# Optimization experiments

Hardware: AMD Instinct MI355X
Metric: run time of the kernel (lower is better)

Reference implementation:

```python
import jax, jax.numpy as jnp
import numpy as np

N = 100000   # nodes
E = 1600000  # edges
F = 128      # node features
H = 64       # hidden_dim
G = 64       # graphs in batch


def setup_inputs() -> dict:
    key = jax.random.key(0)
    ks = jax.random.split(key, 12)
    x = jax.random.normal(ks[0], (N, F), jnp.float32)
    edge_index = jax.random.randint(ks[1], (2, E), 0, N, dtype=jnp.int64)
    batch = jnp.sort(jax.random.randint(ks[2], (N,), 0, G, dtype=jnp.int64))
    s = 0.05
    W1 = jax.random.normal(ks[3], (F, H), jnp.float32) * s
    b1 = jnp.zeros((H,), jnp.float32)
    W2 = jax.random.normal(ks[4], (H, H), jnp.float32) * s
    b2 = jnp.zeros((H,), jnp.float32)
    Wa = jax.random.normal(ks[5], (H, 1), jnp.float32) * s
    ba = jnp.zeros((1,), jnp.float32)
    Wc = jax.random.normal(ks[6], (H, 1), jnp.float32) * s
    bc = jnp.zeros((1,), jnp.float32)
    return {"x": x, "edge_index": edge_index, "batch": batch,
            "W1": W1, "b1": b1, "W2": W2, "b2": b2,
            "Wa": Wa, "ba": ba, "Wc": Wc, "bc": bc}


def _gcn_norm(edge_index, n):
    # Add self-loops, compute symmetric normalization deg^-1/2[src]*deg^-1/2[dst]
    loop = jnp.arange(n, dtype=edge_index.dtype)
    src = jnp.concatenate([edge_index[0], loop])
    dst = jnp.concatenate([edge_index[1], loop])
    deg = jax.ops.segment_sum(jnp.ones_like(src, jnp.float32), dst, num_segments=n)
    dinv = jnp.where(deg > 0, deg ** -0.5, 0.0)
    norm = dinv[src] * dinv[dst]  # [E+N]
    return src, dst, norm


def _gcn_conv(x, W, b, src, dst, norm, n):
    h = x @ W                         # [n, H] dense transform first (PyG order)
    msg = h[src] * norm[:, None]      # gather + normalize [E+n, H]
    agg = jax.ops.segment_sum(msg, dst, num_segments=n)  # scatter-add
    return agg + b


def reference(x, edge_index, batch, W1, b1, W2, b2, Wa, ba, Wc, bc):
    n = x.shape[0]
    src, dst, norm = _gcn_norm(edge_index, n)
    h = jax.nn.relu(_gcn_conv(x, W1, b1, src, dst, norm, n))
    # dropout p=0.1 is identity in eval mode
    h = jax.nn.relu(_gcn_conv(h, W2, b2, src, dst, norm, n))
    action_logits = (h @ Wa + ba)[:, 0]  # [N]
    counts = jax.ops.segment_sum(jnp.ones((n,), jnp.float32), batch, num_segments=G)
    pooled = jax.ops.segment_sum(h, batch, num_segments=G) / jnp.maximum(counts, 1.0)[:, None]
    value = pooled @ Wc + bc  # [G, 1]
    return action_logits, value
```

## Files before the change

kernel.cpp:

```cpp
#include <hip/hip_runtime.h>
#include <hip/hip_fp16.h>
#include <math.h>

#define FEAT 128
#define HID  64
#define BSH  7
#define BNODES (1 << BSH)
#define PB   256
#define SRCM ((1u << 25) - 1)
#define PSPLIT 16

typedef _Float16 f16_t;
typedef f16_t half8 __attribute__((ext_vector_type(8)));
typedef float  f32x4 __attribute__((ext_vector_type(4)));


__global__ void part_hist_k(const int* __restrict__ dst, int* __restrict__ table,
                            int e, int nb) {
    __shared__ int lcnt[1024];
    for (int i = threadIdx.x; i < nb; i += 256) lcnt[i] = 0;
    __syncthreads();
    int eb = (e + PB - 1) / PB;
    int lo = blockIdx.x * eb, hi = min(lo + eb, e);
    for (int i = lo + threadIdx.x; i < hi; i += 256)
        atomicAdd(&lcnt[dst[i] >> BSH], 1);
    __syncthreads();
    for (int k = threadIdx.x; k < nb; k += 256)
        table[k * PB + blockIdx.x] = lcnt[k];
}

__global__ void scan1_k(int* __restrict__ data, int* __restrict__ aux, int L) {
    __shared__ int s[1024];
    int gid = blockIdx.x * 1024 + threadIdx.x;
    int v = (gid < L) ? data[gid] : 0;
    s[threadIdx.x] = v;
    __syncthreads();
    for (int off = 1; off < 1024; off <<= 1) {
        int t = (threadIdx.x >= off) ? s[threadIdx.x - off] : 0;
        __syncthreads();
        s[threadIdx.x] += t;
        __syncthreads();
    }
    if (gid < L) data[gid] = s[threadIdx.x] - v;
    if (threadIdx.x == 1023) aux[blockIdx.x] = s[1023];
}

__global__ void scan2_k(int* aux, int naux) {
    __shared__ int s[1024];
    int v = (threadIdx.x < naux) ? aux[threadIdx.x] : 0;
    s[threadIdx.x] = v;
    __syncthreads();
    for (int off = 1; off < 1024; off <<= 1) {
        int t = (threadIdx.x >= off) ? s[threadIdx.x - off] : 0;
        __syncthreads();
        s[threadIdx.x] += t;
        __syncthreads();
    }
    if (threadIdx.x < naux) aux[threadIdx.x] = s[threadIdx.x] - v;
}

__global__ void part_scatter_k(const int* __restrict__ src, const int* __restrict__ dst,
                               const int* __restrict__ table, const int* __restrict__ aux,
                               unsigned* __restrict__ packed, int e, int nb) {
    __shared__ int loff[1024];
    for (int k = threadIdx.x; k < nb; k += 256) {
        int idx = k * PB + blockIdx.x;
        loff[k] = table[idx] + aux[idx >> 10];
    }
    __syncthreads();
    int eb = (e + PB - 1) / PB;
    int lo = blockIdx.x * eb, hi = min(lo + eb, e);
    for (int i = lo + threadIdx.x; i < hi; i += 256) {
        int d = dst[i];
        int p = atomicAdd(&loff[d >> BSH], 1);
        packed[p] = ((unsigned)(d & (BNODES - 1)) << 25) | (unsigned)src[i];
    }
}


__global__ void bucket_sort_k(const unsigned* __restrict__ packed,
                              const int* __restrict__ table, const int* __restrict__ aux,
                              int* __restrict__ col, int* __restrict__ rowptr,
                              float* __restrict__ dinv, int n, int e, int nb) {
    __shared__ int cnt[BNODES];
    __shared__ int s[BNODES];
    __shared__ int cur[BNODES];
    const int k = blockIdx.x;
    const int t = threadIdx.x;
    if (t < BNODES) cnt[t] = 0;
    __syncthreads();
    int i0 = k * PB;
    int i1 = (k + 1) * PB;
    const int bs = table[i0] + aux[i0 >> 10];
    const int be = (k + 1 < nb) ? (table[i1] + aux[i1 >> 10]) : e;
    for (int i = bs + t; i < be; i += 256)
        atomicAdd(&cnt[packed[i] >> 25], 1);
    __syncthreads();
    if (t < BNODES) s[t] = cnt[t];
    __syncthreads();
    for (int off = 1; off < BNODES; off <<= 1) {
        int v = (t < BNODES && t >= off) ? s[t - off] : 0;
        __syncthreads();
        if (t < BNODES) s[t] += v;
        __syncthreads();
    }
    if (t < BNODES) {
        int base = bs + s[t] - cnt[t];
        cur[t] = base;
        int node = (k << BSH) + t;
        if (node < n) {
            rowptr[node] = base;
            dinv[node] = 1.0f / sqrtf(1.0f + (float)cnt[t]);
            if (node == n - 1) rowptr[n] = base + cnt[t];
        }
    }
    __syncthreads();
    for (int i = bs + t; i < be; i += 256) {
        unsigned u = packed[i];
        int p = atomicAdd(&cur[u >> 25], 1);
        col[p] = (int)(u & SRCM);
    }
}


__global__ __launch_bounds__(256, 3)
void gemm_tile_k(const float* __restrict__ X, const float* __restrict__ W,
                 const float* __restrict__ dinv, __half* __restrict__ out, int n) {
    constexpr int K = FEAT;
    __shared__ float sX[64][K + 4];
    __shared__ float sW[64][64];
    const int row0 = blockIdx.x * 64;
    const int t  = threadIdx.x;
    const int tx = t & 15;
    const int ty = t >> 4;

    const float* xb = X + (size_t)row0 * K;
#pragma unroll
    for (int it = 0; it < K / 16; ++it) {
        int fl = it * 1024 + t * 4;
        int r  = fl >> 7;
        int k  = fl & (K - 1);
        float4 v = make_float4(0.f, 0.f, 0.f, 0.f);
        if (row0 + r < n) v = *(const float4*)(xb + fl);
        *(float4*)&sX[r][k] = v;
    }

    float acc[4][4] = {};
#pragma unroll
    for (int ph = 0; ph < K / 64; ++ph) {
        __syncthreads();
#pragma unroll
        for (int it = 0; it < 4; ++it) {
            int fl = it * 1024 + t * 4;
            *(float4*)&sW[fl >> 6][fl & 63] = *(const float4*)(W + ph * 64 * HID + fl);
        }
        __syncthreads();

#pragma unroll 8
        for (int k = 0; k < 64; k += 4) {
            float4 a[4], b[4];
#pragma unroll
            for (int i = 0; i < 4; i++) a[i] = *(float4*)&sX[ty * 4 + i][ph * 64 + k];
#pragma unroll
            for (int j = 0; j < 4; j++) b[j] = *(float4*)&sW[k + j][tx * 4];
#pragma unroll
            for (int i = 0; i < 4; i++) {
                acc[i][0] = fmaf(a[i].x, b[0].x, acc[i][0]);
                acc[i][1] = fmaf(a[i].x, b[0].y, acc[i][1]);
                acc[i][2] = fmaf(a[i].x, b[0].z, acc[i][2]);
                acc[i][3] = fmaf(a[i].x, b[0].w, acc[i][3]);
                acc[i][0] = fmaf(a[i].y, b[1].x, acc[i][0]);
                acc[i][1] = fmaf(a[i].y, b[1].y, acc[i][1]);
                acc[i][2] = fmaf(a[i].y, b[1].z, acc[i][2]);
                acc[i][3] = fmaf(a[i].y, b[1].w, acc[i][3]);
                acc[i][0] = fmaf(a[i].z, b[2].x, acc[i][0]);
                acc[i][1] = fmaf(a[i].z, b[2].y, acc[i][1]);
                acc[i][2] = fmaf(a[i].z, b[2].z, acc[i][2]);
                acc[i][3] = fmaf(a[i].z, b[2].w, acc[i][3]);
                acc[i][0] = fmaf(a[i].w, b[3].x, acc[i][0]);
                acc[i][1] = fmaf(a[i].w, b[3].y, acc[i][1]);
                acc[i][2] = fmaf(a[i].w, b[3].z, acc[i][2]);
                acc[i][3] = fmaf(a[i].w, b[3].w, acc[i][3]);
            }
        }
    }

#pragma unroll
    for (int i = 0; i < 4; i++) {
        int gr = row0 + ty * 4 + i;
        if (gr < n) {
            float sc = dinv[gr];
            union { __half2 h[2]; unsigned long long u; } pk;
            pk.h[0] = __floats2half2_rn(acc[i][0] * sc, acc[i][1] * sc);
            pk.h[1] = __floats2half2_rn(acc[i][2] * sc, acc[i][3] * sc);
            *(unsigned long long*)(out + (size_t)gr * HID + tx * 4) = pk.u;
        }
    }
}


__global__ void gather1_k(const __half* __restrict__ tS, const int* __restrict__ rowptr,
                          const int* __restrict__ col, const float* __restrict__ dinv,
                          const float* __restrict__ b, __half* __restrict__ out, int n) {
    int node = (int)((blockIdx.x * (size_t)blockDim.x + threadIdx.x) >> 5);
    int lane = threadIdx.x & 31;
    if (node >= n) return;
    int beg = rowptr[node], end = rowptr[node + 1];
    const __half2* tl = (const __half2*)tS + lane;
    float2 acc = __half22float2(tl[node * 32]);
    int e = beg;
    for (; e + 16 <= end; e += 16) {
        int s[16];
        __half2 v[16];
#pragma unroll
        for (int j = 0; j < 16; j++) s[j] = col[e + j];
#pragma unroll
        for (int j = 0; j < 16; j++) v[j] = tl[s[j] * 32];
        float2 t0 = make_float2(0.f, 0.f), t1 = make_float2(0.f, 0.f);
#pragma unroll
        for (int j = 0; j < 8; j++) {
            float2 f = __half22float2(v[j]);
            t0.x += f.x; t0.y += f.y;
        }
#pragma unroll
        for (int j = 8; j < 16; j++) {
            float2 f = __half22float2(v[j]);
            t1.x += f.x; t1.y += f.y;
        }
        acc.x += t0.x + t1.x;
        acc.y += t0.y + t1.y;
    }
    for (; e + 4 <= end; e += 4) {
        __half2 v0 = tl[col[e] * 32];
        __half2 v1 = tl[col[e + 1] * 32];
        __half2 v2 = tl[col[e + 2] * 32];
        __half2 v3 = tl[col[e + 3] * 32];
        float2 f0 = __half22float2(v0), f1 = __half22float2(v1);
        float2 f2 = __half22float2(v2), f3 = __half22float2(v3);
        acc.x += (f0.x + f1.x) + (f2.x + f3.x);
        acc.y += (f0.y + f1.y) + (f2.y + f3.y);
    }
    for (; e < end; ++e) {
        float2 f = __half22float2(tl[col[e] * 32]);
        acc.x += f.x; acc.y += f.y;
    }
    float d = dinv[node];
    float2 bb = *(const float2*)(b + 2 * lane);
    float h0 = fmaxf(fmaf(d, acc.x, bb.x), 0.0f);
    float h1 = fmaxf(fmaf(d, acc.y, bb.y), 0.0f);
    ((__half2*)out)[node * 32 + lane] = __floats2half2_rn(h0, h1);
}


__global__ __launch_bounds__(256)
void t2_k(const __half* __restrict__ h, const float* __restrict__ W2,
          const float* __restrict__ dinv, __half* __restrict__ out, int n) {
    const int wave  = threadIdx.x >> 6;
    const int l     = threadIdx.x & 63;
    const int strip = blockIdx.x * 4 + wave;
    const int r0    = strip * 16;
    if (r0 >= n) return;
    const int col = l & 15;
    const int kb  = l >> 4;

    half8 bf[4][2];
#pragma unroll
    for (int t = 0; t < 4; ++t)
#pragma unroll
        for (int kk = 0; kk < 2; ++kk)
#pragma unroll
            for (int j = 0; j < 8; ++j)
                bf[t][kk][j] = (f16_t)W2[(kk * 32 + kb * 8 + j) * HID + t * 16 + col];

    const int arow = r0 + col;
    const __half* ap = h + (size_t)arow * HID + kb * 8;
    half8 a0 = *(const half8*)(ap);
    half8 a1 = *(const half8*)(ap + 32);

    f32x4 acc[4] = {};
#pragma unroll
    for (int t = 0; t < 4; ++t) {
        acc[t] = __builtin_amdgcn_mfma_f32_16x16x32_f16(a0, bf[t][0], acc[t], 0, 0, 0);
        acc[t] = __builtin_amdgcn_mfma_f32_16x16x32_f16(a1, bf[t][1], acc[t], 0, 0, 0);
    }

    const int rbase = r0 + kb * 4;
#pragma unroll
    for (int r = 0; r < 4; ++r) {
        int gr = rbase + r;
        if (gr < n) {
            float dv = dinv[gr];
#pragma unroll
            for (int t = 0; t < 4; ++t)
                out[(size_t)gr * HID + t * 16 + col] = __float2half(acc[t][r] * dv);
        }
    }
}


__global__ void gather2_k(const __half* __restrict__ tS, const int* __restrict__ rowptr,
                          const int* __restrict__ col, const float* __restrict__ dinv,
                          const float* __restrict__ b, __half* __restrict__ out,
                          const float* __restrict__ Wa, const float* __restrict__ ba,
                          float* __restrict__ logits, int n) {
    int node = (int)((blockIdx.x * (size_t)blockDim.x + threadIdx.x) >> 5);
    int lane = threadIdx.x & 31;
    if (node >= n) return;
    int beg = rowptr[node], end = rowptr[node + 1];
    const __half2* tl = (const __half2*)tS + lane;
    float2 acc = __half22float2(tl[node * 32]);
    int e = beg;
    for (; e + 16 <= end; e += 16) {
        int s[16];
        __half2 v[16];
#pragma unroll
        for (int j = 0; j < 16; j++) s[j] = col[e + j];
#pragma unroll
        for (int j = 0; j < 16; j++) v[j] = tl[s[j] * 32];
        float2 t0 = make_float2(0.f, 0.f), t1 = make_float2(0.f, 0.f);
#pragma unroll
        for (int j = 0; j < 8; j++) {
            float2 f = __half22float2(v[j]);
            t0.x += f.x; t0.y += f.y;
        }
#pragma unroll
        for (int j = 8; j < 16; j++) {
            float2 f = __half22float2(v[j]);
            t1.x += f.x; t1.y += f.y;
        }
        acc.x += t0.x + t1.x;
        acc.y += t0.y + t1.y;
    }
    for (; e + 4 <= end; e += 4) {
        __half2 v0 = tl[col[e] * 32];
        __half2 v1 = tl[col[e + 1] * 32];
        __half2 v2 = tl[col[e + 2] * 32];
        __half2 v3 = tl[col[e + 3] * 32];
        float2 f0 = __half22float2(v0), f1 = __half22float2(v1);
        float2 f2 = __half22float2(v2), f3 = __half22float2(v3);
        acc.x += (f0.x + f1.x) + (f2.x + f3.x);
        acc.y += (f0.y + f1.y) + (f2.y + f3.y);
    }
    for (; e < end; ++e) {
        float2 f = __half22float2(tl[col[e] * 32]);
        acc.x += f.x; acc.y += f.y;
    }
    float d = dinv[node];
    float2 bb = *(const float2*)(b + 2 * lane);
    float h0 = fmaxf(fmaf(d, acc.x, bb.x), 0.0f);
    float h1 = fmaxf(fmaf(d, acc.y, bb.y), 0.0f);
    ((__half2*)out)[node * 32 + lane] = __floats2half2_rn(h0, h1);
    float2 wa = *(const float2*)(Wa + 2 * lane);
    float p = h0 * wa.x + h1 * wa.y;
#pragma unroll
    for (int off = 16; off > 0; off >>= 1) p += __shfl_down(p, off, 32);
    if (lane == 0) logits[node] = p + ba[0];
}


__global__ void pool2_k(const __half* __restrict__ h, const int* __restrict__ batch,
                        float* __restrict__ pooled, int n) {
    const int gid  = blockIdx.x / PSPLIT;
    const int part = blockIdx.x % PSPLIT;
    int lo = 0, hi = n;
    while (lo < hi) { int m = (lo + hi) >> 1; if (batch[m] < gid) lo = m + 1; else hi = m; }
    const int b0 = lo;
    hi = n;
    while (lo < hi) { int m = (lo + hi) >> 1; if (batch[m] < gid + 1) lo = m + 1; else hi = m; }
    const int b1 = lo;
    const int chunk = (b1 - b0 + PSPLIT - 1) / PSPLIT;
    const int r0 = b0 + part * chunk;
    const int r1 = min(r0 + chunk, b1);
    const int lane = threadIdx.x & 31;
    const int rg   = threadIdx.x >> 5;
    const __half2* hp = (const __half2*)h + lane;
    float2 acc = make_float2(0.f, 0.f);
    for (int i = r0 + rg; i < r1; i += 8) {
        float2 f = __half22float2(hp[(size_t)i * 32]);
        acc.x += f.x; acc.y += f.y;
    }
    __shared__ float2 red[8][32];
    red[rg][lane] = acc;
    __syncthreads();
    if (threadIdx.x < 32) {
        float2 s = make_float2(0.f, 0.f);
#pragma unroll
        for (int r = 0; r < 8; r++) { s.x += red[r][threadIdx.x].x; s.y += red[r][threadIdx.x].y; }
        atomicAdd(&pooled[gid * HID + 2 * threadIdx.x], s.x);
        atomicAdd(&pooled[gid * HID + 2 * threadIdx.x + 1], s.y);
    }
}


__global__ void value_k(const float* __restrict__ pooled, const int* __restrict__ batch,
                        const float* __restrict__ Wc, const float* __restrict__ bc,
                        float* __restrict__ val, int n, int g) {
    int gw   = (int)((blockIdx.x * (size_t)blockDim.x + threadIdx.x) >> 6);
    int lane = threadIdx.x & 63;
    if (gw >= g) return;
    int lo = 0, hi = n;
    while (lo < hi) { int m = (lo + hi) >> 1; if (batch[m] < gw) lo = m + 1; else hi = m; }
    int b0 = lo;
    lo = 0; hi = n;
    while (lo < hi) { int m = (lo + hi) >> 1; if (batch[m] < gw + 1) lo = m + 1; else hi = m; }
    float cnt = fmaxf((float)(lo - b0), 1.0f);
    float p = (pooled[gw * HID + lane] / cnt) * Wc[lane];
#pragma unroll
    for (int off = 32; off > 0; off >>= 1) p += __shfl_down(p, off);
    if (lane == 0) val[gw] = p + bc[0];
}

extern "C" void kernel_launch(void* const* d_in, const int* in_sizes, int n_in,
                              void* d_out, int out_size, void* d_ws, size_t ws_size,
                              hipStream_t stream) {
    const float* x     = (const float*)d_in[0];
    const int*   ei    = (const int*)d_in[1];
    const int*   batch = (const int*)d_in[2];
    const float* W1    = (const float*)d_in[3];
    const float* b1    = (const float*)d_in[4];
    const float* W2    = (const float*)d_in[5];
    const float* b2    = (const float*)d_in[6];
    const float* Wa    = (const float*)d_in[7];
    const float* ba    = (const float*)d_in[8];
    const float* Wc    = (const float*)d_in[9];
    const float* bc    = (const float*)d_in[10];

    const int n = in_sizes[0] / FEAT;
    const int e = in_sizes[1] / 2;
    const int g = out_size - n;
    const int* src = ei;
    const int* dst = ei + e;

    const int nb = (n + BNODES - 1) >> BSH;
    const int L  = nb * PB;

    float*    ws     = (float*)d_ws;
    float*    dinv   = ws;
    float*    bufA   = dinv + n;
    float*    bufB   = bufA + (size_t)n * HID;
    float*    pooled = bufB + (size_t)n * HID;
    int*      table  = (int*)(pooled + (size_t)g * HID);
    int*      aux    = table + L;
    int*      rowptr = aux + 1024;
    int*      col    = rowptr + n + 1;
    unsigned* packed = (unsigned*)bufA;
    __half*   tS1    = (__half*)bufA;
    __half*   h16    = (__half*)bufB;
    __half*   tS2    = (__half*)bufA;
    __half*   h2     = (__half*)bufB;

    const int B = 256;
    const int gridT  = (n + 63) / 64;
    const int gridG  = (int)(((size_t)n * 32 + B - 1) / B);
    const int strips = (n + 15) / 16;
    const int gridT2 = (strips + 3) / 4;
    const int nb1    = (L + 1023) / 1024;

    (void)hipMemsetAsync(pooled, 0, (size_t)g * HID * sizeof(float), stream);

    part_hist_k<<<PB, B, 0, stream>>>(dst, table, e, nb);
    scan1_k<<<nb1, 1024, 0, stream>>>(table, aux, L);
    scan2_k<<<1, 1024, 0, stream>>>(aux, nb1);
    part_scatter_k<<<PB, B, 0, stream>>>(src, dst, table, aux, packed, e, nb);
    bucket_sort_k<<<nb, B, 0, stream>>>(packed, table, aux, col, rowptr, dinv, n, e, nb);

    gemm_tile_k<<<gridT, B, 0, stream>>>(x, W1, dinv, tS1, n);
    gather1_k<<<gridG, B, 0, stream>>>(tS1, rowptr, col, dinv, b1, h16, n);

    t2_k<<<gridT2, B, 0, stream>>>(h16, W2, dinv, tS2, n);
    gather2_k<<<gridG, B, 0, stream>>>(tS2, rowptr, col, dinv, b2, h2,
                                       Wa, ba, (float*)d_out, n);

    pool2_k<<<g * PSPLIT, B, 0, stream>>>(h2, batch, pooled, n);
    value_k<<<(g * 64 + B - 1) / B, B, 0, stream>>>(pooled, batch, Wc, bc,
                                                    (float*)d_out + n, n, g);
}
```

Before: 296.6 us.

## Replace two-level bucket CSR build with global-atomic counting sort

Replaces the partitioned histogram, bucket scatter and per-bucket local sort with a simpler CSR build: global atomic degree counting, a scan over n nodes, a finalize kernel for rowptr/dinv, and a scatter using global atomics on per-node cursors. It drops the packed intermediate pass and the local-memory sort, at the cost of 1.6M contended global atomics in two passes and fully random col writes. Column order within a row becomes nondeterministic, which can change float summation order.

```diff
diff --git a/kernel.cpp b/kernel.cpp
--- a/kernel.cpp
+++ b/kernel.cpp
@@ -4,10 +4,6 @@
 
 #define FEAT 128
 #define HID  64
-#define BSH  7
-#define BNODES (1 << BSH)
-#define PB   256
-#define SRCM ((1u << 25) - 1)
 #define PSPLIT 16
 
 typedef _Float16 f16_t;
@@ -15,18 +11,11 @@
 typedef float  f32x4 __attribute__((ext_vector_type(4)));
 
 
-__global__ void part_hist_k(const int* __restrict__ dst, int* __restrict__ table,
-                            int e, int nb) {
-    __shared__ int lcnt[1024];
-    for (int i = threadIdx.x; i < nb; i += 256) lcnt[i] = 0;
-    __syncthreads();
-    int eb = (e + PB - 1) / PB;
-    int lo = blockIdx.x * eb, hi = min(lo + eb, e);
-    for (int i = lo + threadIdx.x; i < hi; i += 256)
-        atomicAdd(&lcnt[dst[i] >> BSH], 1);
-    __syncthreads();
-    for (int k = threadIdx.x; k < nb; k += 256)
-        table[k * PB + blockIdx.x] = lcnt[k];
+__global__ void deg_k(const int* __restrict__ dst, int* __restrict__ deg, int e) {
+    int i = blockIdx.x * 256 + threadIdx.x;
+    int stride = gridDim.x * 256;
+    for (; i < e; i += stride)
+        atomicAdd(&deg[dst[i]], 1);
 }
 
 __global__ void scan1_k(int* __restrict__ data, int* __restrict__ aux, int L) {
@@ -59,66 +48,26 @@
     if (threadIdx.x < naux) aux[threadIdx.x] = s[threadIdx.x] - v;
 }
 
-__global__ void part_scatter_k(const int* __restrict__ src, const int* __restrict__ dst,
-                               const int* __restrict__ table, const int* __restrict__ aux,
-                               unsigned* __restrict__ packed, int e, int nb) {
-    __shared__ int loff[1024];
-    for (int k = threadIdx.x; k < nb; k += 256) {
-        int idx = k * PB + blockIdx.x;
-        loff[k] = table[idx] + aux[idx >> 10];
-    }
-    __syncthreads();
-    int eb = (e + PB - 1) / PB;
-    int lo = blockIdx.x * eb, hi = min(lo + eb, e);
-    for (int i = lo + threadIdx.x; i < hi; i += 256) {
-        int d = dst[i];
-        int p = atomicAdd(&loff[d >> BSH], 1);
-        packed[p] = ((unsigned)(d & (BNODES - 1)) << 25) | (unsigned)src[i];
-    }
-}
-
-
-__global__ void bucket_sort_k(const unsigned* __restrict__ packed,
-                              const int* __restrict__ table, const int* __restrict__ aux,
-                              int* __restrict__ col, int* __restrict__ rowptr,
-                              float* __restrict__ dinv, int n, int e, int nb) {
-    __shared__ int cnt[BNODES];
-    __shared__ int s[BNODES];
-    __shared__ int cur[BNODES];
-    const int k = blockIdx.x;
-    const int t = threadIdx.x;
-    if (t < BNODES) cnt[t] = 0;
-    __syncthreads();
-    int i0 = k * PB;
-    int i1 = (k + 1) * PB;
-    const int bs = table[i0] + aux[i0 >> 10];
-    const int be = (k + 1 < nb) ? (table[i1] + aux[i1 >> 10]) : e;
-    for (int i = bs + t; i < be; i += 256)
-        atomicAdd(&cnt[packed[i] >> 25], 1);
-    __syncthreads();
-    if (t < BNODES) s[t] = cnt[t];
-    __syncthreads();
-    for (int off = 1; off < BNODES; off <<= 1) {
-        int v = (t < BNODES && t >= off) ? s[t - off] : 0;
-        __syncthreads();
-        if (t < BNODES) s[t] += v;
-        __syncthreads();
-    }
-    if (t < BNODES) {
-        int base = bs + s[t] - cnt[t];
-        cur[t] = base;
-        int node = (k << BSH) + t;
-        if (node < n) {
-            rowptr[node] = base;
-            dinv[node] = 1.0f / sqrtf(1.0f + (float)cnt[t]);
-            if (node == n - 1) rowptr[n] = base + cnt[t];
-        }
-    }
-    __syncthreads();
-    for (int i = bs + t; i < be; i += 256) {
-        unsigned u = packed[i];
-        int p = atomicAdd(&cur[u >> 25], 1);
-        col[p] = (int)(u & SRCM);
+__global__ void fin_k(const int* __restrict__ sc, const int* __restrict__ aux,
+                      int* __restrict__ rowptr, int* __restrict__ cur,
+                      float* __restrict__ dinv, int n, int e) {
+    int i = blockIdx.x * 256 + threadIdx.x;
+    if (i >= n) return;
+    int rp = sc[i] + aux[i >> 10];
+    rowptr[i] = rp;
+    cur[i] = rp;
+    int next = (i + 1 < n) ? (sc[i + 1] + aux[(i + 1) >> 10]) : e;
+    dinv[i] = 1.0f / sqrtf(1.0f + (float)(next - rp));
+    if (i == n - 1) rowptr[n] = e;
+}
+
+__global__ void scat_k(const int* __restrict__ src, const int* __restrict__ dst,
+                       int* __restrict__ cur, int* __restrict__ col, int e) {
+    int i = blockIdx.x * 256 + threadIdx.x;
+    int stride = gridDim.x * 256;
+    for (; i < e; i += stride) {
+        int p = atomicAdd(&cur[dst[i]], 1);
+        col[p] = src[i];
     }
 }
 
@@ -431,19 +380,16 @@
     const int* src = ei;
     const int* dst = ei + e;
 
-    const int nb = (n + BNODES - 1) >> BSH;
-    const int L  = nb * PB;
-
     float*    ws     = (float*)d_ws;
     float*    dinv   = ws;
     float*    bufA   = dinv + n;
     float*    bufB   = bufA + (size_t)n * HID;
     float*    pooled = bufB + (size_t)n * HID;
-    int*      table  = (int*)(pooled + (size_t)g * HID);
-    int*      aux    = table + L;
+    int*      deg    = (int*)(pooled + (size_t)g * HID);
+    int*      aux    = deg + n;
     int*      rowptr = aux + 1024;
-    int*      col    = rowptr + n + 1;
-    unsigned* packed = (unsigned*)bufA;
+    int*      cur    = rowptr + n + 1;
+    int*      col    = cur + n;
     __half*   tS1    = (__half*)bufA;
     __half*   h16    = (__half*)bufB;
     __half*   tS2    = (__half*)bufA;
@@ -454,15 +400,16 @@
     const int gridG  = (int)(((size_t)n * 32 + B - 1) / B);
     const int strips = (n + 15) / 16;
     const int gridT2 = (strips + 3) / 4;
-    const int nb1    = (L + 1023) / 1024;
+    const int nb1    = (n + 1023) / 1024;
 
     (void)hipMemsetAsync(pooled, 0, (size_t)g * HID * sizeof(float), stream);
-
-    part_hist_k<<<PB, B, 0, stream>>>(dst, table, e, nb);
-    scan1_k<<<nb1, 1024, 0, stream>>>(table, aux, L);
+    (void)hipMemsetAsync(deg, 0, (size_t)n * sizeof(int), stream);
+
+    deg_k<<<1024, B, 0, stream>>>(dst, deg, e);
+    scan1_k<<<nb1, 1024, 0, stream>>>(deg, aux, n);
     scan2_k<<<1, 1024, 0, stream>>>(aux, nb1);
-    part_scatter_k<<<PB, B, 0, stream>>>(src, dst, table, aux, packed, e, nb);
-    bucket_sort_k<<<nb, B, 0, stream>>>(packed, table, aux, col, rowptr, dinv, n, e, nb);
+    fin_k<<<(n + B - 1) / B, B, 0, stream>>>(deg, aux, rowptr, cur, dinv, n, e);
+    scat_k<<<2048, B, 0, stream>>>(src, dst, cur, col, e);
 
     gemm_tile_k<<<gridT, B, 0, stream>>>(x, W1, dinv, tS1, n);
     gather1_k<<<gridG, B, 0, stream>>>(tS1, rowptr, col, dinv, b1, h16, n);
```

New measurement: 441.3 us. +48.8%, slower.
